# Kernel optimization log

Measured on AMD Instinct MI355X. Metric: run time of the kernel, lower is better.

The kernel has to match this reference:

```python
import jax, jax.numpy as jnp
import numpy as np

INPUT_DIM = 24
HIDDEN = 128
NUM_LAYERS = 3
OUTPUT_DIM = 1


def _lstm_layer(x, Wih, Whh, bih, bhh):
    """Single LSTM layer, PyTorch gate order (i, f, g, o). x: [B,T,D] -> [B,T,H]."""
    B = x.shape[0]
    H = Whh.shape[1]
    # Precompute input projections for all timesteps at once: [B,T,4H]
    xg = jnp.einsum('btd,gd->btg', x, Wih) + bih
    xg = jnp.swapaxes(xg, 0, 1)  # [T,B,4H]
    h0 = jnp.zeros((B, H), x.dtype)
    c0 = jnp.zeros((B, H), x.dtype)

    def step(carry, xt):
        h, c = carry
        gates = xt + h @ Whh.T + bhh  # [B,4H]
        i, f, g, o = jnp.split(gates, 4, axis=-1)
        i = jax.nn.sigmoid(i)
        f = jax.nn.sigmoid(f)
        g = jnp.tanh(g)
        o = jax.nn.sigmoid(o)
        c = f * c + i * g
        h = o * jnp.tanh(c)
        return (h, c), h

    _, hs = jax.lax.scan(step, (h0, c0), xg)  # hs: [T,B,H]
    return jnp.swapaxes(hs, 0, 1)  # [B,T,H]


def setup_inputs() -> dict:
    key = jax.random.key(0)
    ks = jax.random.split(key, 16)
    B, T = 2048, 256
    s = 0.05
    inp = {
        'x': jax.random.normal(ks[0], (B, T, INPUT_DIM), dtype=jnp.float32),
    }
    dims_in = [INPUT_DIM, HIDDEN, HIDDEN]
    for l in range(NUM_LAYERS):
        inp[f'Wih{l}'] = jax.random.normal(ks[1 + 4 * l], (4 * HIDDEN, dims_in[l]), dtype=jnp.float32) * s
        inp[f'Whh{l}'] = jax.random.normal(ks[2 + 4 * l], (4 * HIDDEN, HIDDEN), dtype=jnp.float32) * s
        inp[f'bih{l}'] = jax.random.normal(ks[3 + 4 * l], (4 * HIDDEN,), dtype=jnp.float32) * s
        inp[f'bhh{l}'] = jax.random.normal(ks[4 + 4 * l], (4 * HIDDEN,), dtype=jnp.float32) * s
    inp['Wfc'] = jax.random.normal(ks[13], (OUTPUT_DIM, HIDDEN), dtype=jnp.float32) * s
    inp['bfc'] = jax.random.normal(ks[14], (OUTPUT_DIM,), dtype=jnp.float32) * s
    return inp


def reference(x, Wih0, Whh0, bih0, bhh0, Wih1, Whh1, bih1, bhh1,
              Wih2, Whh2, bih2, bhh2, Wfc, bfc):
    # 3 stacked LSTM layers (dropout inactive in eval mode), zero initial state.
    h = _lstm_layer(x, Wih0, Whh0, bih0, bhh0)
    h = _lstm_layer(h, Wih1, Whh1, bih1, bhh1)
    h = _lstm_layer(h, Wih2, Whh2, bih2, bhh2)
    # Linear projection of the final timestep: [B,1]
    return h[:, -1, :] @ Wfc.T + bfc
```

## Files before the change

kernel.cpp:

```cpp
#include <hip/hip_runtime.h>

#define T_STEPS 256
#define BATCH   2048
#define HID     128
#define ROWS    8
#define BH      (BATCH * HID)

typedef short short8  __attribute__((ext_vector_type(8)));
typedef float float4v __attribute__((ext_vector_type(4)));

template<int P> struct IntC { static constexpr int value = P; };

__device__ __forceinline__ unsigned short f2bf(float f) {
    unsigned int u = __builtin_bit_cast(unsigned int, f);
    u += 0x7fffu + ((u >> 16) & 1u);
    return (unsigned short)(u >> 16);
}
__device__ __forceinline__ float bf2f(unsigned short b) {
    unsigned int u = ((unsigned int)b) << 16;
    return __builtin_bit_cast(float, u);
}

#if __has_builtin(__builtin_amdgcn_exp2f)
#define EXP2F(x) __builtin_amdgcn_exp2f(x)
#else
#define EXP2F(x) exp2f(x)
#endif
__device__ __forceinline__ float sigf(float x) {
    return __builtin_amdgcn_rcpf(1.0f + EXP2F(x * -1.442695041f));
}
__device__ __forceinline__ float tanh_fast(float x) {
    return 2.0f * __builtin_amdgcn_rcpf(1.0f + EXP2F(x * -2.885390082f)) - 1.0f;
}

__device__ __forceinline__ void block_sync_lds() {
    asm volatile("s_waitcnt lgkmcnt(0)" ::: "memory");
    __builtin_amdgcn_s_barrier();
    __builtin_amdgcn_sched_barrier(0);
}

__device__ __forceinline__ int lposH(int row, int off) {
    return row * 256 + (off ^ ((row & 7) << 4));
}
__device__ __forceinline__ int lposX(int row, int off) {
    return row * 256 + (off ^ ((row & 7) << 4));
}
__device__ __forceinline__ int lposX0(int row, int off) {
    return row * 64 + (off ^ ((row & 3) << 4));
}

__device__ __forceinline__ short8 load_w8(const float* __restrict__ p) {
    float4v a = *reinterpret_cast<const float4v*>(p);
    float4v b = *reinterpret_cast<const float4v*>(p + 4);
    short8 r;
    r[0] = (short)f2bf(a[0]); r[1] = (short)f2bf(a[1]);
    r[2] = (short)f2bf(a[2]); r[3] = (short)f2bf(a[3]);
    r[4] = (short)f2bf(b[0]); r[5] = (short)f2bf(b[1]);
    r[6] = (short)f2bf(b[2]); r[7] = (short)f2bf(b[3]);
    return r;
}

#define LDS_BYTES 12288

template<bool IS_L0, bool WRITE_H, bool FINAL>
__device__ __forceinline__ void lstm_phase(
    unsigned char* a_lds,
    const float* __restrict__ x0,
    const float* __restrict__ Wih,
    const float* __restrict__ Whh,
    const float* __restrict__ bih,
    const float* __restrict__ bhh,
    unsigned short* __restrict__ hbuf,
    const float* __restrict__ Wfc,
    const float* __restrict__ bfc,
    float* __restrict__ out,
    const int tid, const int b0)
{
    constexpr int XKS = IS_L0 ? 1 : 4;
    constexpr int XRB = IS_L0 ? 64 : 256;
    constexpr int HB  = ROWS * 256;
    constexpr int XB  = 16 * XRB;
    const int XS0 = 2 * HB, XS1 = 2 * HB + XB;

    const int lane = tid & 63;
    const int wv   = tid >> 6;

    const int t16   = lane & 15;
    const int kgrp8 = (lane >> 4) * 8;
    const int jcol  = 16 * wv + t16;
    const int row0  = ((lane >> 4) & 1) * 4 + ((lane >> 5) & 1) * 2;

    const int g2   = t16 >> 2;
    const int hrow = ((g2 & 1) << 2) | ((g2 >> 1) << 1) | (t16 & 1);
    int aoffH[4];
    #pragma unroll
    for (int ks = 0; ks < 4; ++ks)
        aoffH[ks] = lposH(hrow, ks * 64 + kgrp8 * 2);
    int aoffX[XKS];
    #pragma unroll
    for (int s = 0; s < XKS; ++s)
        aoffX[s] = IS_L0 ? lposX0(t16, kgrp8 * 2)
                         : lposX(t16, s * 64 + kgrp8 * 2);

    const int hwoff0 = lposH(row0,     2 * jcol);
    const int hwoff1 = lposH(row0 + 1, 2 * jcol);

    const int sh_row = (tid >> 5) & 7, sh_c8 = tid & 31;
    const int hroff8 = lposH(sh_row, sh_c8 * 8);
    const size_t sgoff8 = (size_t)(b0 + sh_row) * HID + sh_c8 * 4;

    const int tid2 = tid & 255;
    const int sar = tid2 >> 4, sc16 = tid2 & 15;
    const int sb  = (sar & 1) | (((sar >> 3) & 1) << 1) | (((sar >> 2) & 1) << 2);
    const int ss  = (sar >> 1) & 1;
    const int xwoff = lposX(sar, sc16 * 16);
    const size_t xgrow = (size_t)(b0 + sb) * HID + sc16 * 8;
    const bool xvalid = (sc16 < 12);
    const int xw0off = lposX0(sar, sc16 * 4);
    const size_t x0row = (size_t)(b0 + sb) * (T_STEPS * 24) + sc16 * 2;

    short8 wfh[4][4], wfx[4][XKS];
    float  bias[4];
    #pragma unroll
    for (int q = 0; q < 4; ++q) {
        const int n = 128 * q + jcol;
        bias[q] = bih[n] + bhh[n];
        #pragma unroll
        for (int ks = 0; ks < 4; ++ks)
            wfh[q][ks] = load_w8(Whh + n * 128 + ks * 32 + kgrp8);
        if (IS_L0) {
            if (kgrp8 < 24) wfx[q][0] = load_w8(Wih + n * 24 + kgrp8);
            else            { short8 z = {0,0,0,0,0,0,0,0}; wfx[q][0] = z; }
        } else {
            #pragma unroll
            for (int s = 0; s < 4; ++s)
                wfx[q][s] = load_w8(Wih + n * 128 + s * 32 + kgrp8);
        }
    }

    {
        short8 z = {0,0,0,0,0,0,0,0};
        #pragma unroll
        for (int i = 0; i < 2; ++i) {
            const int a = tid * 16 + i * 8192;
            if (a < LDS_BYTES)
                *reinterpret_cast<short8*>(&a_lds[a]) = z;
        }
    }
    __syncthreads();

    short8 xpre = {0,0,0,0,0,0,0,0};
    float2 xpf  = {0.f, 0.f};
    if (tid >= 256) {
        if (!IS_L0) {
            short8 v0 = *reinterpret_cast<const short8*>(&hbuf[(size_t)(0 + ss) * BH + xgrow]);
            short8 v1 = *reinterpret_cast<const short8*>(&hbuf[(size_t)(2 + ss) * BH + xgrow]);
            *reinterpret_cast<short8*>(&a_lds[XS0 + xwoff]) = v0;
            *reinterpret_cast<short8*>(&a_lds[XS1 + xwoff]) = v1;
            xpre = *reinterpret_cast<const short8*>(&hbuf[(size_t)(4 + ss) * BH + xgrow]);
        } else if (xvalid) {
            float2 a = *reinterpret_cast<const float2*>(&x0[x0row + (size_t)(0 + ss) * 24]);
            float2 b = *reinterpret_cast<const float2*>(&x0[x0row + (size_t)(2 + ss) * 24]);
            unsigned int pa, pb;
            asm("v_cvt_pk_bf16_f32 %0, %1, %2" : "=v"(pa) : "v"(a.x), "v"(a.y));
            asm("v_cvt_pk_bf16_f32 %0, %1, %2" : "=v"(pb) : "v"(b.x), "v"(b.y));
            *reinterpret_cast<unsigned int*>(&a_lds[XS0 + xw0off]) = pa;
            *reinterpret_cast<unsigned int*>(&a_lds[XS1 + xw0off]) = pb;
            xpf = *reinterpret_cast<const float2*>(&x0[x0row + (size_t)(4 + ss) * 24]);
        }
    }
    __syncthreads();

    float4v xgA[4], xgB[4];
    #pragma unroll
    for (int q = 0; q < 4; ++q) {
        xgA[q] = float4v{bias[q], bias[q], bias[q], bias[q]};
        xgB[q] = float4v{bias[q], bias[q], bias[q], bias[q]};
    }
    {
        short8 xa[XKS];
        #pragma unroll
        for (int s = 0; s < XKS; ++s)
            xa[s] = *reinterpret_cast<const short8*>(&a_lds[XS0 + aoffX[s]]);
        #pragma unroll
        for (int s = 0; s < XKS; ++s)
            #pragma unroll
            for (int q = 0; q < 4; ++q)
                xgA[q] = __builtin_amdgcn_mfma_f32_16x16x32_bf16(xa[s], wfx[q][s], xgA[q], 0, 0, 0);
    }

    float creg[2] = {0.f, 0.f};

    auto do_step = [&](int t, auto PC) {
        constexpr int POS = decltype(PC)::value;
        constexpr bool EVEN = (POS & 1) == 0;
        const int rb = EVEN ? 0 : HB;
        const int wb = EVEN ? HB : 0;
        float4v (&cons)[4] = (POS < 2) ? xgA : xgB;
        float4v (&bld)[4]  = (POS < 2) ? xgB : xgA;
        const int XRD = (POS < 2) ? XS1 : XS0;
        const int XWR = (POS == 1) ? XS0 : XS1;

        short8 hva[4];
        #pragma unroll
        for (int ks = 0; ks < 4; ++ks)
            hva[ks] = *reinterpret_cast<const short8*>(&a_lds[rb + aoffH[ks]]);
        float4v acc[4];
        #pragma unroll
        for (int q = 0; q < 4; ++q) {
            const float a = EVEN ? cons[q][0] : cons[q][2];
            const float b = EVEN ? cons[q][1] : cons[q][3];
            acc[q] = float4v{a, b, a, b};
        }
        if (tid < 256) {
            if (WRITE_H && t > 0) {
                int2 hv = *reinterpret_cast<const int2*>(&a_lds[rb + hroff8]);
                *reinterpret_cast<int2*>(&hbuf[(size_t)(t - 1) * BH + sgoff8]) = hv;
            }
        } else {
            if constexpr (EVEN) {
                int tl = t + 4 + ss;
                tl = (tl < T_STEPS) ? tl : (T_STEPS - 1);
                if constexpr (!IS_L0) {
                    xpre = *reinterpret_cast<const short8*>(&hbuf[(size_t)tl * BH + xgrow]);
                } else {
                    if (xvalid)
                        xpf = *reinterpret_cast<const float2*>(&x0[x0row + (size_t)tl * 24]);
                }
            } else {
                if constexpr (!IS_L0) {
                    *reinterpret_cast<short8*>(&a_lds[XWR + xwoff]) = xpre;
                } else {
                    if (xvalid) {
                        unsigned int p;
                        asm("v_cvt_pk_bf16_f32 %0, %1, %2" : "=v"(p) : "v"(xpf.x), "v"(xpf.y));
                        *reinterpret_cast<unsigned int*>(&a_lds[XWR + xw0off]) = p;
                    }
                }
            }
        }
        __builtin_amdgcn_s_setprio(1);
        #pragma unroll
        for (int ks = 0; ks < 4; ++ks)
            #pragma unroll
            for (int q = 0; q < 4; ++q)
                acc[q] = __builtin_amdgcn_mfma_f32_16x16x32_bf16(hva[ks], wfh[q][ks], acc[q], 0, 0, 0);
        __builtin_amdgcn_s_setprio(0);
        {
            const float c0 = sigf(acc[1][0]) * creg[0] + sigf(acc[0][0]) * tanh_fast(acc[2][0]);
            const float c1 = sigf(acc[1][1]) * creg[1] + sigf(acc[0][1]) * tanh_fast(acc[2][1]);
            creg[0] = c0;  creg[1] = c1;
            const float h0 = sigf(acc[3][0]) * tanh_fast(c0);
            const float h1 = sigf(acc[3][1]) * tanh_fast(c1);
            unsigned int packed;
            asm("v_cvt_pk_bf16_f32 %0, %1, %2" : "=v"(packed) : "v"(h0), "v"(h1));
            *reinterpret_cast<unsigned short*>(&a_lds[wb + hwoff0]) =
                (unsigned short)(packed & 0xffffu);
            *reinterpret_cast<unsigned short*>(&a_lds[wb + hwoff1]) =
                (unsigned short)(packed >> 16);
        }
        if constexpr (!IS_L0) {
            if constexpr (EVEN) {
                short8 xa0 = *reinterpret_cast<const short8*>(&a_lds[XRD + aoffX[0]]);
                short8 xa1 = *reinterpret_cast<const short8*>(&a_lds[XRD + aoffX[1]]);
                #pragma unroll
                for (int q = 0; q < 4; ++q)
                    bld[q] = float4v{bias[q], bias[q], bias[q], bias[q]};
                #pragma unroll
                for (int q = 0; q < 4; ++q)
                    bld[q] = __builtin_amdgcn_mfma_f32_16x16x32_bf16(xa0, wfx[q][0], bld[q], 0, 0, 0);
                #pragma unroll
                for (int q = 0; q < 4; ++q)
                    bld[q] = __builtin_amdgcn_mfma_f32_16x16x32_bf16(xa1, wfx[q][1], bld[q], 0, 0, 0);
            } else {
                short8 xa2 = *reinterpret_cast<const short8*>(&a_lds[XRD + aoffX[2]]);
                short8 xa3 = *reinterpret_cast<const short8*>(&a_lds[XRD + aoffX[3]]);
                #pragma unroll
                for (int q = 0; q < 4; ++q)
                    bld[q] = __builtin_amdgcn_mfma_f32_16x16x32_bf16(xa2, wfx[q][2], bld[q], 0, 0, 0);
                #pragma unroll
                for (int q = 0; q < 4; ++q)
                    bld[q] = __builtin_amdgcn_mfma_f32_16x16x32_bf16(xa3, wfx[q][3], bld[q], 0, 0, 0);
            }
        } else {
            if constexpr (EVEN) {
                short8 xa0 = *reinterpret_cast<const short8*>(&a_lds[XRD + aoffX[0]]);
                #pragma unroll
                for (int q = 0; q < 4; ++q)
                    bld[q] = float4v{bias[q], bias[q], bias[q], bias[q]};
                #pragma unroll
                for (int q = 0; q < 4; ++q)
                    bld[q] = __builtin_amdgcn_mfma_f32_16x16x32_bf16(xa0, wfx[q][0], bld[q], 0, 0, 0);
            }
        }
        block_sync_lds();
    };

    for (int m = 0; m < T_STEPS / 4; ++m) {
        const int t0 = 4 * m;
        do_step(t0,     IntC<0>{});
        do_step(t0 + 1, IntC<1>{});
        do_step(t0 + 2, IntC<2>{});
        do_step(t0 + 3, IntC<3>{});
    }
    if (WRITE_H && tid < 256) {
        int2 hv = *reinterpret_cast<const int2*>(&a_lds[0 + hroff8]);
        *reinterpret_cast<int2*>(&hbuf[(size_t)(T_STEPS - 1) * BH + sgoff8]) = hv;
    }
    if (FINAL && tid < 128) {
        const int r = tid >> 4, seg = tid & 15;
        float s = 0.f;
        #pragma unroll
        for (int k = 0; k < 8; ++k) {
            const int j = seg * 8 + k;
            s += bf2f(*reinterpret_cast<const unsigned short*>(&a_lds[lposH(r, 2 * j)]))
                 * Wfc[j];
        }
        #pragma unroll
        for (int off = 8; off >= 1; off >>= 1) s += __shfl_xor(s, off);
        if (seg == 0) out[b0 + r] = s + bfc[0];
    }
}

__global__ __launch_bounds__(512, 2)
void lstm3(const float* __restrict__ x0,
           const float* __restrict__ Wih0, const float* __restrict__ Whh0,
           const float* __restrict__ bih0, const float* __restrict__ bhh0,
           const float* __restrict__ Wih1, const float* __restrict__ Whh1,
           const float* __restrict__ bih1, const float* __restrict__ bhh1,
           const float* __restrict__ Wih2, const float* __restrict__ Whh2,
           const float* __restrict__ bih2, const float* __restrict__ bhh2,
           const float* __restrict__ Wfc,  const float* __restrict__ bfc,
           unsigned short* __restrict__ hbuf, float* __restrict__ out)
{
    __shared__ __attribute__((aligned(16))) unsigned char a_lds[LDS_BYTES];
    const int tid = threadIdx.x;
    const int b0  = blockIdx.x * ROWS;

    lstm_phase<true,  true,  false>(a_lds, x0, Wih0, Whh0, bih0, bhh0, hbuf,
                                    nullptr, nullptr, nullptr, tid, b0);
    __syncthreads();
    lstm_phase<false, true,  false>(a_lds, nullptr, Wih1, Whh1, bih1, bhh1, hbuf,
                                    nullptr, nullptr, nullptr, tid, b0);
    __syncthreads();
    lstm_phase<false, false, true >(a_lds, nullptr, Wih2, Whh2, bih2, bhh2, hbuf,
                                    Wfc, bfc, out, tid, b0);
}

extern "C" void kernel_launch(void* const* d_in, const int* in_sizes, int n_in,
                              void* d_out, int out_size, void* d_ws, size_t ws_size,
                              hipStream_t stream) {
    (void)in_sizes; (void)n_in; (void)out_size; (void)ws_size;
    const float* x    = (const float*)d_in[0];
    const float* Wih0 = (const float*)d_in[1];
    const float* Whh0 = (const float*)d_in[2];
    const float* bih0 = (const float*)d_in[3];
    const float* bhh0 = (const float*)d_in[4];
    const float* Wih1 = (const float*)d_in[5];
    const float* Whh1 = (const float*)d_in[6];
    const float* bih1 = (const float*)d_in[7];
    const float* bhh1 = (const float*)d_in[8];
    const float* Wih2 = (const float*)d_in[9];
    const float* Whh2 = (const float*)d_in[10];
    const float* bih2 = (const float*)d_in[11];
    const float* bhh2 = (const float*)d_in[12];
    const float* Wfc  = (const float*)d_in[13];
    const float* bfc  = (const float*)d_in[14];
    float* out = (float*)d_out;
    unsigned short* hbuf = (unsigned short*)d_ws;

    dim3 grid(BATCH / ROWS), block(512);
    lstm3<<<grid, block, 0, stream>>>(x, Wih0, Whh0, bih0, bhh0,
                                      Wih1, Whh1, bih1, bhh1,
                                      Wih2, Whh2, bih2, bhh2,
                                      Wfc, bfc, hbuf, out);
}
```

Before: 573.4 us.

## Warp-specialize LSTM: split recurrent and input-projection waves via LDS staging

Splits the 512-thread block into four waves doing only the recurrent h@Whh MFMAs and gate math over 32 hidden columns each, and four waves computing the input projection and publishing it to LDS a step ahead. The goal is to take input-projection MFMAs and global prefetch off the serial recurrent path. In exchange each recurrent wave does twice the MFMAs per step, and LDS use rises sharply to stage the projected gates.

```diff
diff --git a/kernel.cpp b/kernel.cpp
--- a/kernel.cpp
+++ b/kernel.cpp
@@ -3,13 +3,10 @@
 #define T_STEPS 256
 #define BATCH   2048
 #define HID     128
-#define ROWS    8
 #define BH      (BATCH * HID)
 
 typedef short short8  __attribute__((ext_vector_type(8)));
 typedef float float4v __attribute__((ext_vector_type(4)));
-
-template<int P> struct IntC { static constexpr int value = P; };
 
 __device__ __forceinline__ unsigned short f2bf(float f) {
     unsigned int u = __builtin_bit_cast(unsigned int, f);
@@ -60,7 +57,7 @@
     return r;
 }
 
-#define LDS_BYTES 12288
+#define LDS_BYTES 77824
 
 template<bool IS_L0, bool WRITE_H, bool FINAL>
 __device__ __forceinline__ void lstm_phase(
@@ -78,235 +75,300 @@
 {
     constexpr int XKS = IS_L0 ? 1 : 4;
     constexpr int XRB = IS_L0 ? 64 : 256;
-    constexpr int HB  = ROWS * 256;
+    constexpr int HB  = 2048;
     constexpr int XB  = 16 * XRB;
-    const int XS0 = 2 * HB, XS1 = 2 * HB + XB;
-
-    const int lane = tid & 63;
-    const int wv   = tid >> 6;
-
+    constexpr int SL0 = 2 * HB;
+    constexpr int SL1 = 2 * HB + XB;
+    constexpr int XGB = 2 * HB + 2 * XB;
+    constexpr int PARS  = 16384;
+    constexpr int PAIRS = 32768;
+
+    const int lane  = tid & 63;
+    const int wv    = tid >> 6;
     const int t16   = lane & 15;
     const int kgrp8 = (lane >> 4) * 8;
-    const int jcol  = 16 * wv + t16;
+    const bool upper = lane >= 32;
     const int row0  = ((lane >> 4) & 1) * 4 + ((lane >> 5) & 1) * 2;
-
-    const int g2   = t16 >> 2;
-    const int hrow = ((g2 & 1) << 2) | ((g2 >> 1) << 1) | (t16 & 1);
-    int aoffH[4];
-    #pragma unroll
-    for (int ks = 0; ks < 4; ++ks)
-        aoffH[ks] = lposH(hrow, ks * 64 + kgrp8 * 2);
-    int aoffX[XKS];
-    #pragma unroll
-    for (int s = 0; s < XKS; ++s)
-        aoffX[s] = IS_L0 ? lposX0(t16, kgrp8 * 2)
-                         : lposX(t16, s * 64 + kgrp8 * 2);
-
-    const int hwoff0 = lposH(row0,     2 * jcol);
-    const int hwoff1 = lposH(row0 + 1, 2 * jcol);
-
-    const int sh_row = (tid >> 5) & 7, sh_c8 = tid & 31;
-    const int hroff8 = lposH(sh_row, sh_c8 * 8);
-    const size_t sgoff8 = (size_t)(b0 + sh_row) * HID + sh_c8 * 4;
-
-    const int tid2 = tid & 255;
-    const int sar = tid2 >> 4, sc16 = tid2 & 15;
-    const int sb  = (sar & 1) | (((sar >> 3) & 1) << 1) | (((sar >> 2) & 1) << 2);
-    const int ss  = (sar >> 1) & 1;
-    const int xwoff = lposX(sar, sc16 * 16);
-    const size_t xgrow = (size_t)(b0 + sb) * HID + sc16 * 8;
-    const bool xvalid = (sc16 < 12);
-    const int xw0off = lposX0(sar, sc16 * 4);
-    const size_t x0row = (size_t)(b0 + sb) * (T_STEPS * 24) + sc16 * 2;
-
-    short8 wfh[4][4], wfx[4][XKS];
-    float  bias[4];
-    #pragma unroll
-    for (int q = 0; q < 4; ++q) {
-        const int n = 128 * q + jcol;
-        bias[q] = bih[n] + bhh[n];
-        #pragma unroll
-        for (int ks = 0; ks < 4; ++ks)
-            wfh[q][ks] = load_w8(Whh + n * 128 + ks * 32 + kgrp8);
-        if (IS_L0) {
-            if (kgrp8 < 24) wfx[q][0] = load_w8(Wih + n * 24 + kgrp8);
-            else            { short8 z = {0,0,0,0,0,0,0,0}; wfx[q][0] = z; }
-        } else {
-            #pragma unroll
-            for (int s = 0; s < 4; ++s)
-                wfx[q][s] = load_w8(Wih + n * 128 + s * 32 + kgrp8);
-        }
-    }
 
     {
         short8 z = {0,0,0,0,0,0,0,0};
-        #pragma unroll
-        for (int i = 0; i < 2; ++i) {
-            const int a = tid * 16 + i * 8192;
-            if (a < LDS_BYTES)
-                *reinterpret_cast<short8*>(&a_lds[a]) = z;
-        }
+        for (int a = tid * 16; a < 2 * HB + 2 * XB; a += 512 * 16)
+            *reinterpret_cast<short8*>(&a_lds[a]) = z;
     }
     __syncthreads();
 
-    short8 xpre = {0,0,0,0,0,0,0,0};
-    float2 xpf  = {0.f, 0.f};
-    if (tid >= 256) {
-        if (!IS_L0) {
+    if (tid < 256) {
+        const int jA = 32 * wv + t16, jB = jA + 16;
+        const int g2 = t16 >> 2;
+        const int hrow = ((g2 & 1) << 2) | ((g2 >> 1) << 1) | (t16 & 1);
+        int aoffH[4];
+        #pragma unroll
+        for (int ks = 0; ks < 4; ++ks)
+            aoffH[ks] = lposH(hrow, ks * 64 + kgrp8 * 2);
+        int hst[2][2];
+        hst[0][0] = lposH(row0,     2 * jA);
+        hst[0][1] = lposH(row0 + 1, 2 * jA);
+        hst[1][0] = lposH(row0,     2 * jB);
+        hst[1][1] = lposH(row0 + 1, 2 * jB);
+        int xgr[2][4];
+        #pragma unroll
+        for (int c = 0; c < 2; ++c)
+            #pragma unroll
+            for (int q = 0; q < 4; ++q)
+                xgr[c][q] = XGB + ((q * 128 + (c ? jB : jA)) * 8 + row0) * 4;
+
+        short8 wfh[2][4][4];
+        #pragma unroll
+        for (int c = 0; c < 2; ++c)
+            #pragma unroll
+            for (int q = 0; q < 4; ++q) {
+                const int n = 128 * q + (c ? jB : jA);
+                #pragma unroll
+                for (int ks = 0; ks < 4; ++ks)
+                    wfh[c][q][ks] = load_w8(Whh + n * 128 + ks * 32 + kgrp8);
+            }
+
+        float crA0 = 0.f, crA1 = 0.f, crB0 = 0.f, crB1 = 0.f;
+        block_sync_lds();
+        block_sync_lds();
+
+        auto hstep = [&](const int rb, const int wb, const int xgo) {
+            short8 hva[4];
+            #pragma unroll
+            for (int ks = 0; ks < 4; ++ks)
+                hva[ks] = *reinterpret_cast<const short8*>(&a_lds[rb + aoffH[ks]]);
+            float2 xg[2][4];
+            #pragma unroll
+            for (int c = 0; c < 2; ++c)
+                #pragma unroll
+                for (int q = 0; q < 4; ++q)
+                    xg[c][q] = *reinterpret_cast<const float2*>(&a_lds[xgo + xgr[c][q]]);
+            float4v acc[2][4];
+            #pragma unroll
+            for (int c = 0; c < 2; ++c)
+                #pragma unroll
+                for (int q = 0; q < 4; ++q)
+                    acc[c][q] = float4v{xg[c][q].x, xg[c][q].y, xg[c][q].x, xg[c][q].y};
+            __builtin_amdgcn_s_setprio(1);
+            #pragma unroll
+            for (int ks = 0; ks < 4; ++ks)
+                #pragma unroll
+                for (int c = 0; c < 2; ++c)
+                    #pragma unroll
+                    for (int q = 0; q < 4; ++q)
+                        acc[c][q] = __builtin_amdgcn_mfma_f32_16x16x32_bf16(
+                            hva[ks], wfh[c][q][ks], acc[c][q], 0, 0, 0);
+            __builtin_amdgcn_s_setprio(0);
+            {
+                const float i0 = upper ? acc[0][0][2] : acc[0][0][0];
+                const float i1 = upper ? acc[0][0][3] : acc[0][0][1];
+                const float f0 = upper ? acc[0][1][2] : acc[0][1][0];
+                const float f1 = upper ? acc[0][1][3] : acc[0][1][1];
+                const float g0 = upper ? acc[0][2][2] : acc[0][2][0];
+                const float g1 = upper ? acc[0][2][3] : acc[0][2][1];
+                const float o0 = upper ? acc[0][3][2] : acc[0][3][0];
+                const float o1 = upper ? acc[0][3][3] : acc[0][3][1];
+                const float c0 = sigf(f0) * crA0 + sigf(i0) * tanh_fast(g0);
+                const float c1 = sigf(f1) * crA1 + sigf(i1) * tanh_fast(g1);
+                crA0 = c0;  crA1 = c1;
+                const float h0 = sigf(o0) * tanh_fast(c0);
+                const float h1 = sigf(o1) * tanh_fast(c1);
+                unsigned int pk;
+                asm("v_cvt_pk_bf16_f32 %0, %1, %2" : "=v"(pk) : "v"(h0), "v"(h1));
+                *reinterpret_cast<unsigned short*>(&a_lds[wb + hst[0][0]]) =
+                    (unsigned short)(pk & 0xffffu);
+                *reinterpret_cast<unsigned short*>(&a_lds[wb + hst[0][1]]) =
+                    (unsigned short)(pk >> 16);
+            }
+            {
+                const float i0 = upper ? acc[1][0][2] : acc[1][0][0];
+                const float i1 = upper ? acc[1][0][3] : acc[1][0][1];
+                const float f0 = upper ? acc[1][1][2] : acc[1][1][0];
+                const float f1 = upper ? acc[1][1][3] : acc[1][1][1];
+                const float g0 = upper ? acc[1][2][2] : acc[1][2][0];
+                const float g1 = upper ? acc[1][2][3] : acc[1][2][1];
+                const float o0 = upper ? acc[1][3][2] : acc[1][3][0];
+                const float o1 = upper ? acc[1][3][3] : acc[1][3][1];
+                const float c0 = sigf(f0) * crB0 + sigf(i0) * tanh_fast(g0);
+                const float c1 = sigf(f1) * crB1 + sigf(i1) * tanh_fast(g1);
+                crB0 = c0;  crB1 = c1;
+                const float h0 = sigf(o0) * tanh_fast(c0);
+                const float h1 = sigf(o1) * tanh_fast(c1);
+                unsigned int pk;
+                asm("v_cvt_pk_bf16_f32 %0, %1, %2" : "=v"(pk) : "v"(h0), "v"(h1));
+                *reinterpret_cast<unsigned short*>(&a_lds[wb + hst[1][0]]) =
+                    (unsigned short)(pk & 0xffffu);
+                *reinterpret_cast<unsigned short*>(&a_lds[wb + hst[1][1]]) =
+                    (unsigned short)(pk >> 16);
+            }
+            block_sync_lds();
+        };
+
+        for (int mm = 0; mm < T_STEPS / 4; ++mm) {
+            hstep(0,  HB, 0);
+            hstep(HB, 0,  PARS);
+            hstep(0,  HB, PAIRS);
+            hstep(HB, 0,  PAIRS + PARS);
+        }
+    } else {
+        const int jA = 32 * (wv - 4) + t16, jB = jA + 16;
+        const int tid2 = tid & 255;
+        const int sh_row = tid2 >> 5, sh_c8 = tid2 & 31;
+        const int hroff8 = lposH(sh_row, sh_c8 * 8);
+        const size_t sgoff8 = (size_t)(b0 + sh_row) * HID + sh_c8 * 4;
+        const int sar = tid2 >> 4, sc16 = tid2 & 15;
+        const int sb  = (sar & 1) | (((sar >> 3) & 1) << 1) | (((sar >> 2) & 1) << 2);
+        const int ss  = (sar >> 1) & 1;
+        const int xwoff = lposX(sar, sc16 * 16);
+        const size_t xgrow = (size_t)(b0 + sb) * HID + sc16 * 8;
+        const bool xvalid = sc16 < 12;
+        const int xw0off = lposX0(sar, sc16 * 4);
+        const size_t x0row = (size_t)(b0 + sb) * (T_STEPS * 24) + sc16 * 2;
+        int aoffX[XKS];
+        #pragma unroll
+        for (int s = 0; s < XKS; ++s)
+            aoffX[s] = IS_L0 ? lposX0(t16, kgrp8 * 2)
+                             : lposX(t16, s * 64 + kgrp8 * 2);
+        int xgw[2][4];
+        #pragma unroll
+        for (int c = 0; c < 2; ++c)
+            #pragma unroll
+            for (int q = 0; q < 4; ++q)
+                xgw[c][q] = XGB + ((q * 128 + (c ? jB : jA)) * 8 + row0) * 4;
+
+        short8 wfx[2][4][XKS];
+        float  bias[2][4];
+        #pragma unroll
+        for (int c = 0; c < 2; ++c)
+            #pragma unroll
+            for (int q = 0; q < 4; ++q) {
+                const int n = 128 * q + (c ? jB : jA);
+                bias[c][q] = bih[n] + bhh[n];
+                if constexpr (IS_L0) {
+                    if (kgrp8 < 24) wfx[c][q][0] = load_w8(Wih + n * 24 + kgrp8);
+                    else { short8 z = {0,0,0,0,0,0,0,0}; wfx[c][q][0] = z; }
+                } else {
+                    #pragma unroll
+                    for (int s = 0; s < 4; ++s)
+                        wfx[c][q][s] = load_w8(Wih + n * 128 + s * 32 + kgrp8);
+                }
+            }
+
+        if constexpr (!IS_L0) {
             short8 v0 = *reinterpret_cast<const short8*>(&hbuf[(size_t)(0 + ss) * BH + xgrow]);
             short8 v1 = *reinterpret_cast<const short8*>(&hbuf[(size_t)(2 + ss) * BH + xgrow]);
-            *reinterpret_cast<short8*>(&a_lds[XS0 + xwoff]) = v0;
-            *reinterpret_cast<short8*>(&a_lds[XS1 + xwoff]) = v1;
-            xpre = *reinterpret_cast<const short8*>(&hbuf[(size_t)(4 + ss) * BH + xgrow]);
+            *reinterpret_cast<short8*>(&a_lds[SL0 + xwoff]) = v0;
+            *reinterpret_cast<short8*>(&a_lds[SL1 + xwoff]) = v1;
         } else if (xvalid) {
             float2 a = *reinterpret_cast<const float2*>(&x0[x0row + (size_t)(0 + ss) * 24]);
             float2 b = *reinterpret_cast<const float2*>(&x0[x0row + (size_t)(2 + ss) * 24]);
             unsigned int pa, pb;
             asm("v_cvt_pk_bf16_f32 %0, %1, %2" : "=v"(pa) : "v"(a.x), "v"(a.y));
             asm("v_cvt_pk_bf16_f32 %0, %1, %2" : "=v"(pb) : "v"(b.x), "v"(b.y));
-            *reinterpret_cast<unsigned int*>(&a_lds[XS0 + xw0off]) = pa;
-            *reinterpret_cast<unsigned int*>(&a_lds[XS1 + xw0off]) = pb;
-            xpf = *reinterpret_cast<const float2*>(&x0[x0row + (size_t)(4 + ss) * 24]);
+            *reinterpret_cast<unsigned int*>(&a_lds[SL0 + xw0off]) = pa;
+            *reinterpret_cast<unsigned int*>(&a_lds[SL1 + xw0off]) = pb;
+        }
+        block_sync_lds();
+
+        float4v xacc[2][4];
+        auto xinit = [&]() {
+            #pragma unroll
+            for (int c = 0; c < 2; ++c)
+                #pragma unroll
+                for (int q = 0; q < 4; ++q)
+                    xacc[c][q] = float4v{bias[c][q], bias[c][q], bias[c][q], bias[c][q]};
+        };
+        auto xmfma2 = [&](const int SLrd, const int s0) {
+            short8 a0 = *reinterpret_cast<const short8*>(&a_lds[SLrd + aoffX[s0]]);
+            short8 a1 = *reinterpret_cast<const short8*>(&a_lds[SLrd + aoffX[s0 + 1]]);
+            #pragma unroll
+            for (int c = 0; c < 2; ++c)
+                #pragma unroll
+                for (int q = 0; q < 4; ++q)
+                    xacc[c][q] = __builtin_amdgcn_mfma_f32_16x16x32_bf16(
+                        a0, wfx[c][q][s0], xacc[c][q], 0, 0, 0);
+            #pragma unroll
+            for (int c = 0; c < 2; ++c)
+                #pragma unroll
+                for (int q = 0; q < 4; ++q)
+                    xacc[c][q] = __builtin_amdgcn_mfma_f32_16x16x32_bf16(
+                        a1, wfx[c][q][s0 + 1], xacc[c][q], 0, 0, 0);
+        };
+        auto xmfma1 = [&](const int SLrd) {
+            short8 a0 = *reinterpret_cast<const short8*>(&a_lds[SLrd + aoffX[0]]);
+            #pragma unroll
+            for (int c = 0; c < 2; ++c)
+                #pragma unroll
+                for (int q = 0; q < 4; ++q)
+                    xacc[c][q] = __builtin_amdgcn_mfma_f32_16x16x32_bf16(
+                        a0, wfx[c][q][0], xacc[c][q], 0, 0, 0);
+        };
+        auto xgwrite = [&](const int XGP) {
+            #pragma unroll
+            for (int c = 0; c < 2; ++c)
+                #pragma unroll
+                for (int q = 0; q < 4; ++q) {
+                    float2 lo = {xacc[c][q][0], xacc[c][q][1]};
+                    float2 hi = {xacc[c][q][2], xacc[c][q][3]};
+                    *reinterpret_cast<float2*>(&a_lds[XGP + xgw[c][q]]) = lo;
+                    *reinterpret_cast<float2*>(&a_lds[XGP + PARS + xgw[c][q]]) = hi;
+                }
+        };
+
+        xinit();
+        if constexpr (!IS_L0) { xmfma2(SL0, 0); xmfma2(SL0, 2); }
+        else xmfma1(SL0);
+        xgwrite(0);
+        block_sync_lds();
+
+        short8 xpre = {0,0,0,0,0,0,0,0};
+        float2 xpf  = {0.f, 0.f};
+
+        auto xstepE = [&](int t, const int SLrd) {
+            if (WRITE_H && t > 0) {
+                int2 hv = *reinterpret_cast<const int2*>(&a_lds[0 + hroff8]);
+                *reinterpret_cast<int2*>(&hbuf[(size_t)(t - 1) * BH + sgoff8]) = hv;
+            }
+            int tl = t + 4 + ss;  tl = tl < T_STEPS ? tl : T_STEPS - 1;
+            if constexpr (!IS_L0)
+                xpre = *reinterpret_cast<const short8*>(&hbuf[(size_t)tl * BH + xgrow]);
+            else if (xvalid)
+                xpf = *reinterpret_cast<const float2*>(&x0[x0row + (size_t)tl * 24]);
+            xinit();
+            if constexpr (!IS_L0) xmfma2(SLrd, 0);
+            else xmfma1(SLrd);
+            block_sync_lds();
+        };
+        auto xstepO = [&](int t, const int SLrd, const int SLwr, const int XGP) {
+            if (WRITE_H) {
+                int2 hv = *reinterpret_cast<const int2*>(&a_lds[HB + hroff8]);
+                *reinterpret_cast<int2*>(&hbuf[(size_t)(t - 1) * BH + sgoff8]) = hv;
+            }
+            if constexpr (!IS_L0)
+                *reinterpret_cast<short8*>(&a_lds[SLwr + xwoff]) = xpre;
+            else if (xvalid) {
+                unsigned int p;
+                asm("v_cvt_pk_bf16_f32 %0, %1, %2" : "=v"(p) : "v"(xpf.x), "v"(xpf.y));
+                *reinterpret_cast<unsigned int*>(&a_lds[SLwr + xw0off]) = p;
+            }
+            if constexpr (!IS_L0) xmfma2(SLrd, 2);
+            xgwrite(XGP);
+            block_sync_lds();
+        };
+
+        for (int mm = 0; mm < T_STEPS / 4; ++mm) {
+            const int t0 = 4 * mm;
+            xstepE(t0,     SL1);
+            xstepO(t0 + 1, SL1, SL0, PAIRS);
+            xstepE(t0 + 2, SL0);
+            xstepO(t0 + 3, SL0, SL1, 0);
+        }
+        if (WRITE_H) {
+            int2 hv = *reinterpret_cast<const int2*>(&a_lds[0 + hroff8]);
+            *reinterpret_cast<int2*>(&hbuf[(size_t)(T_STEPS - 1) * BH + sgoff8]) = hv;
         }
     }
-    __syncthreads();
-
-    float4v xgA[4], xgB[4];
-    #pragma unroll
-    for (int q = 0; q < 4; ++q) {
-        xgA[q] = float4v{bias[q], bias[q], bias[q], bias[q]};
-        xgB[q] = float4v{bias[q], bias[q], bias[q], bias[q]};
-    }
-    {
-        short8 xa[XKS];
-        #pragma unroll
-        for (int s = 0; s < XKS; ++s)
-            xa[s] = *reinterpret_cast<const short8*>(&a_lds[XS0 + aoffX[s]]);
-        #pragma unroll
-        for (int s = 0; s < XKS; ++s)
-            #pragma unroll
-            for (int q = 0; q < 4; ++q)
-                xgA[q] = __builtin_amdgcn_mfma_f32_16x16x32_bf16(xa[s], wfx[q][s], xgA[q], 0, 0, 0);
-    }
-
-    float creg[2] = {0.f, 0.f};
-
-    auto do_step = [&](int t, auto PC) {
-        constexpr int POS = decltype(PC)::value;
-        constexpr bool EVEN = (POS & 1) == 0;
-        const int rb = EVEN ? 0 : HB;
-        const int wb = EVEN ? HB : 0;
-        float4v (&cons)[4] = (POS < 2) ? xgA : xgB;
-        float4v (&bld)[4]  = (POS < 2) ? xgB : xgA;
-        const int XRD = (POS < 2) ? XS1 : XS0;
-        const int XWR = (POS == 1) ? XS0 : XS1;
-
-        short8 hva[4];
-        #pragma unroll
-        for (int ks = 0; ks < 4; ++ks)
-            hva[ks] = *reinterpret_cast<const short8*>(&a_lds[rb + aoffH[ks]]);
-        float4v acc[4];
-        #pragma unroll
-        for (int q = 0; q < 4; ++q) {
-            const float a = EVEN ? cons[q][0] : cons[q][2];
-            const float b = EVEN ? cons[q][1] : cons[q][3];
-            acc[q] = float4v{a, b, a, b};
-        }
-        if (tid < 256) {
-            if (WRITE_H && t > 0) {
-                int2 hv = *reinterpret_cast<const int2*>(&a_lds[rb + hroff8]);
-                *reinterpret_cast<int2*>(&hbuf[(size_t)(t - 1) * BH + sgoff8]) = hv;
-            }
-        } else {
-            if constexpr (EVEN) {
-                int tl = t + 4 + ss;
-                tl = (tl < T_STEPS) ? tl : (T_STEPS - 1);
-                if constexpr (!IS_L0) {
-                    xpre = *reinterpret_cast<const short8*>(&hbuf[(size_t)tl * BH + xgrow]);
-                } else {
-                    if (xvalid)
-                        xpf = *reinterpret_cast<const float2*>(&x0[x0row + (size_t)tl * 24]);
-                }
-            } else {
-                if constexpr (!IS_L0) {
-                    *reinterpret_cast<short8*>(&a_lds[XWR + xwoff]) = xpre;
-                } else {
-                    if (xvalid) {
-                        unsigned int p;
-                        asm("v_cvt_pk_bf16_f32 %0, %1, %2" : "=v"(p) : "v"(xpf.x), "v"(xpf.y));
-                        *reinterpret_cast<unsigned int*>(&a_lds[XWR + xw0off]) = p;
-                    }
-                }
-            }
-        }
-        __builtin_amdgcn_s_setprio(1);
-        #pragma unroll
-        for (int ks = 0; ks < 4; ++ks)
-            #pragma unroll
-            for (int q = 0; q < 4; ++q)
-                acc[q] = __builtin_amdgcn_mfma_f32_16x16x32_bf16(hva[ks], wfh[q][ks], acc[q], 0, 0, 0);
-        __builtin_amdgcn_s_setprio(0);
-        {
-            const float c0 = sigf(acc[1][0]) * creg[0] + sigf(acc[0][0]) * tanh_fast(acc[2][0]);
-            const float c1 = sigf(acc[1][1]) * creg[1] + sigf(acc[0][1]) * tanh_fast(acc[2][1]);
-            creg[0] = c0;  creg[1] = c1;
-            const float h0 = sigf(acc[3][0]) * tanh_fast(c0);
-            const float h1 = sigf(acc[3][1]) * tanh_fast(c1);
-            unsigned int packed;
-            asm("v_cvt_pk_bf16_f32 %0, %1, %2" : "=v"(packed) : "v"(h0), "v"(h1));
-            *reinterpret_cast<unsigned short*>(&a_lds[wb + hwoff0]) =
-                (unsigned short)(packed & 0xffffu);
-            *reinterpret_cast<unsigned short*>(&a_lds[wb + hwoff1]) =
-                (unsigned short)(packed >> 16);
-        }
-        if constexpr (!IS_L0) {
-            if constexpr (EVEN) {
-                short8 xa0 = *reinterpret_cast<const short8*>(&a_lds[XRD + aoffX[0]]);
-                short8 xa1 = *reinterpret_cast<const short8*>(&a_lds[XRD + aoffX[1]]);
-                #pragma unroll
-                for (int q = 0; q < 4; ++q)
-                    bld[q] = float4v{bias[q], bias[q], bias[q], bias[q]};
-                #pragma unroll
-                for (int q = 0; q < 4; ++q)
-                    bld[q] = __builtin_amdgcn_mfma_f32_16x16x32_bf16(xa0, wfx[q][0], bld[q], 0, 0, 0);
-                #pragma unroll
-                for (int q = 0; q < 4; ++q)
-                    bld[q] = __builtin_amdgcn_mfma_f32_16x16x32_bf16(xa1, wfx[q][1], bld[q], 0, 0, 0);
-            } else {
-                short8 xa2 = *reinterpret_cast<const short8*>(&a_lds[XRD + aoffX[2]]);
-                short8 xa3 = *reinterpret_cast<const short8*>(&a_lds[XRD + aoffX[3]]);
-                #pragma unroll
-                for (int q = 0; q < 4; ++q)
-                    bld[q] = __builtin_amdgcn_mfma_f32_16x16x32_bf16(xa2, wfx[q][2], bld[q], 0, 0, 0);
-                #pragma unroll
-                for (int q = 0; q < 4; ++q)
-                    bld[q] = __builtin_amdgcn_mfma_f32_16x16x32_bf16(xa3, wfx[q][3], bld[q], 0, 0, 0);
-            }
-        } else {
-            if constexpr (EVEN) {
-                short8 xa0 = *reinterpret_cast<const short8*>(&a_lds[XRD + aoffX[0]]);
-                #pragma unroll
-                for (int q = 0; q < 4; ++q)
-                    bld[q] = float4v{bias[q], bias[q], bias[q], bias[q]};
-                #pragma unroll
-                for (int q = 0; q < 4; ++q)
-                    bld[q] = __builtin_amdgcn_mfma_f32_16x16x32_bf16(xa0, wfx[q][0], bld[q], 0, 0, 0);
-            }
-        }
-        block_sync_lds();
-    };
-
-    for (int m = 0; m < T_STEPS / 4; ++m) {
-        const int t0 = 4 * m;
-        do_step(t0,     IntC<0>{});
-        do_step(t0 + 1, IntC<1>{});
-        do_step(t0 + 2, IntC<2>{});
-        do_step(t0 + 3, IntC<3>{});
-    }
-    if (WRITE_H && tid < 256) {
-        int2 hv = *reinterpret_cast<const int2*>(&a_lds[0 + hroff8]);
-        *reinterpret_cast<int2*>(&hbuf[(size_t)(T_STEPS - 1) * BH + sgoff8]) = hv;
-    }
+
     if (FINAL && tid < 128) {
         const int r = tid >> 4, seg = tid & 15;
         float s = 0.f;
@@ -335,7 +397,7 @@
 {
     __shared__ __attribute__((aligned(16))) unsigned char a_lds[LDS_BYTES];
     const int tid = threadIdx.x;
-    const int b0  = blockIdx.x * ROWS;
+    const int b0  = blockIdx.x * 8;
 
     lstm_phase<true,  true,  false>(a_lds, x0, Wih0, Whh0, bih0, bhh0, hbuf,
                                     nullptr, nullptr, nullptr, tid, b0);
@@ -369,7 +431,7 @@
     float* out = (float*)d_out;
     unsigned short* hbuf = (unsigned short*)d_ws;
 
-    dim3 grid(BATCH / ROWS), block(512);
+    dim3 grid(BATCH / 8), block(512);
     lstm3<<<grid, block, 0, stream>>>(x, Wih0, Whh0, bih0, bhh0,
                                       Wih1, Whh1, bih1, bhh1,
                                       Wih2, Whh2, bih2, bhh2,
```

Result: slower. 678.1 us (+18.3%).
